# Performance work log

Hardware: AMD Instinct MI355X
Metric: run time of the kernel (lower is better)

Reference implementation:

```python
import jax, jax.numpy as jnp
import numpy as np

NUM_HEADS = 4

def setup_inputs() -> dict:
    key = jax.random.key(0)
    ks = jax.random.split(key, 7)
    B, Lq, Lk, E, D, LAT = 16, 256, 4096, 64, 32, 32
    query = jax.random.normal(ks[0], (B, Lq, E), dtype=jnp.float32)
    key_in = jax.random.normal(ks[1], (B, Lk, E), dtype=jnp.float32)
    value = jax.random.normal(ks[2], (B, Lk, D), dtype=jnp.float32)
    mask = jax.random.randint(ks[3], (B, Lk, D), 0, 2, dtype=jnp.int32)
    Wq = jax.random.normal(ks[4], (E, E), dtype=jnp.float32) / np.sqrt(E).astype(np.float32)
    bq = jnp.zeros((E,), dtype=jnp.float32)
    Wk = jax.random.normal(ks[5], (E, E), dtype=jnp.float32) / np.sqrt(E).astype(np.float32)
    bk = jnp.zeros((E,), dtype=jnp.float32)
    Wo = jax.random.normal(ks[6], (NUM_HEADS * D, LAT), dtype=jnp.float32) / np.sqrt(NUM_HEADS * D).astype(np.float32)
    bo = jnp.zeros((LAT,), dtype=jnp.float32)
    return {"query": query, "key": key_in, "value": value, "mask": mask,
            "Wq": Wq, "bq": bq, "Wk": Wk, "bk": bk, "Wo": Wo, "bo": bo}

def reference(query, key, value, mask, Wq, bq, Wk, bk, Wo, bo):
    B, Lk, D = value.shape
    Lq = query.shape[1]
    h = NUM_HEADS
    ek = query.shape[-1] // h  # embed_time_k
    # linear maps (torch Linear: y = x @ W; here W stored as (in, out))
    q = (query @ Wq + bq).reshape(B, Lq, h, ek).transpose(0, 2, 1, 3)  # (B,h,Lq,ek)
    k = (key @ Wk + bk).reshape(B, Lk, h, ek).transpose(0, 2, 1, 3)    # (B,h,Lk,ek)
    scores = jnp.einsum('bhqe,bhke->bhqk', q, k) / jnp.sqrt(jnp.asarray(ek, q.dtype))
    # Original repeats scores over D, masks per-feature with -inf, softmaxes over Lk,
    # then does a weighted sum. Equivalent fused form (never builds (B,h,Lq,Lk,D)):
    e = jnp.exp(scores - jnp.max(scores, axis=-1, keepdims=True))  # (B,h,Lq,Lk)
    m = mask.astype(value.dtype)                                   # (B,Lk,D) 0/1
    num = jnp.einsum('bhqk,bkd->bhqd', e, m * value)
    den = jnp.einsum('bhqk,bkd->bhqd', e, m)
    x = num / den                                                  # (B,h,Lq,D)
    x = x.transpose(0, 2, 1, 3).reshape(B, Lq, h * D)
    return x @ Wo + bo  # (B, Lq, latent_dim)
```

## Files before the change

kernel.cpp:

```cpp
#include <hip/hip_runtime.h>
#include <hip/hip_bf16.h>
#include <math.h>

typedef __bf16 bf16;
typedef bf16 bf16x2 __attribute__((ext_vector_type(2)));
typedef bf16 bf16x4 __attribute__((ext_vector_type(4)));
typedef bf16 bf16x8 __attribute__((ext_vector_type(8)));
typedef float f32x4 __attribute__((ext_vector_type(4)));
typedef float f32x16 __attribute__((ext_vector_type(16)));
typedef unsigned int u32x2 __attribute__((ext_vector_type(2)));
typedef unsigned int u32x4 __attribute__((ext_vector_type(4)));

#define B_   16
#define LQ_  256
#define LK_  4096
#define E_   64
#define H_   4
#define EK_  16
#define D_   32
#define LAT_ 32

#define OFF_QP    0u
#define OFF_KP    524288u
#define OFF_MVFB  8912896u
#define OFF_WOT   17301504u
#define OFF_NDP   17309696u
#define WS_NEED   50864128u

#define LOG2E 1.44269504f

__device__ inline f32x4 mfma_bf16(bf16x8 a, bf16x8 b, f32x4 c) {
  return __builtin_amdgcn_mfma_f32_16x16x32_bf16(a, b, c, 0, 0, 0);
}
__device__ inline f32x16 mfma_bf16_32(bf16x8 a, bf16x8 b, f32x16 c) {
  return __builtin_amdgcn_mfma_f32_32x32x16_bf16(a, b, c, 0, 0, 0);
}

__device__ inline void pl32swap(unsigned &a, unsigned &b) {
#if __has_builtin(__builtin_amdgcn_permlane32_swap)
  u32x2 r = __builtin_amdgcn_permlane32_swap(a, b, false, false);
  a = r[0]; b = r[1];
#else
  asm volatile("v_permlane32_swap_b32 %0, %1" : "+v"(a), "+v"(b));
#endif
}

__global__ __launch_bounds__(256) void prep_kernel(
    const float* __restrict__ query, const float* __restrict__ key,
    const float* __restrict__ value, const int* __restrict__ mask,
    const float* __restrict__ Wq, const float* __restrict__ bq,
    const float* __restrict__ Wk, const float* __restrict__ bk,
    const float* __restrict__ Wo,
    bf16* __restrict__ qp, bf16* __restrict__ kp,
    bf16* __restrict__ mvfB, bf16* __restrict__ WoT)
{
  __shared__ __align__(16) bf16 s_b[16896];
  const int bid = blockIdx.x;
  const int tid = threadIdx.x;

  if (bid < 544) {
    const bool isQ = bid < 32;
    const int row0 = isQ ? bid * 128 : (bid - 32) * 128;
    const float* in   = isQ ? query : key;
    const float* W    = isQ ? Wq : Wk;
    const float* bias = isQ ? bq : bk;
    bf16* outp        = isQ ? qp : kp;
    const float scal  = isQ ? (0.25f * LOG2E) : 1.0f;

    bf16* sIn = s_b;
    bf16* sWT = s_b + 9216;

#pragma unroll
    for (int p = 0; p < 8; ++p) {
      int f4 = tid + p * 256;
      int row = f4 >> 4, e4 = (f4 & 15) * 4;
      float4 v = *(const float4*)(in + (size_t)(row0 + row) * 64 + e4);
      bf16x4 b4;
      b4[0] = (bf16)v.x; b4[1] = (bf16)v.y; b4[2] = (bf16)v.z; b4[3] = (bf16)v.w;
      *(bf16x4*)(sIn + row * 72 + e4) = b4;
    }
#pragma unroll
    for (int p = 0; p < 4; ++p) {
      int f4 = tid + p * 256;
      int k = f4 >> 4, c4 = (f4 & 15) * 4;
      float4 v = *(const float4*)(W + k * 64 + c4);
      sWT[(c4 + 0) * 72 + k] = (bf16)v.x;
      sWT[(c4 + 1) * 72 + k] = (bf16)v.y;
      sWT[(c4 + 2) * 72 + k] = (bf16)v.z;
      sWT[(c4 + 3) * 72 + k] = (bf16)v.w;
    }
    __syncthreads();

    const int w = tid >> 6, l = tid & 63, l15 = l & 15, g = l >> 4;
    f32x4 acc[2][4];
#pragma unroll
    for (int mt = 0; mt < 2; ++mt)
#pragma unroll
      for (int nt = 0; nt < 4; ++nt) acc[mt][nt] = f32x4{0.f, 0.f, 0.f, 0.f};

#pragma unroll
    for (int ks = 0; ks < 2; ++ks) {
      bf16x8 A0 = *(bf16x8*)(sIn + (32 * w + l15) * 72 + 32 * ks + 8 * g);
      bf16x8 A1 = *(bf16x8*)(sIn + (32 * w + 16 + l15) * 72 + 32 * ks + 8 * g);
#pragma unroll
      for (int nt = 0; nt < 4; ++nt) {
        bf16x8 Bf = *(bf16x8*)(sWT + (16 * nt + l15) * 72 + 32 * ks + 8 * g);
        acc[0][nt] = mfma_bf16(A0, Bf, acc[0][nt]);
        acc[1][nt] = mfma_bf16(A1, Bf, acc[1][nt]);
      }
    }
#pragma unroll
    for (int mt = 0; mt < 2; ++mt)
#pragma unroll
      for (int nt = 0; nt < 4; ++nt) {
        int col = 16 * nt + l15;
        float bv = bias[col];
#pragma unroll
        for (int r = 0; r < 4; ++r) {
          int row = row0 + 32 * w + 16 * mt + 4 * g + r;
          outp[(size_t)row * 64 + col] = (bf16)((acc[mt][nt][r] + bv) * scal);
        }
      }
  } else if (bid < 800) {
    const int rb = bid - 544;
    const int b = rb >> 4, kk0 = (rb & 15) * 256;
#pragma unroll
    for (int p = 0; p < 8; ++p) {
      int f4 = tid + p * 256;
      int kk = f4 >> 3, d4 = (f4 & 7) * 4;
      size_t gi = ((size_t)(b * LK_ + kk0 + kk)) * 32 + d4;
      float4 v = *(const float4*)(value + gi);
      int4   m = *(const int4*)(mask + gi);
      s_b[(d4 + 0) * 264 + kk] = (bf16)(m.x ? v.x : 0.0f);
      s_b[(d4 + 1) * 264 + kk] = (bf16)(m.y ? v.y : 0.0f);
      s_b[(d4 + 2) * 264 + kk] = (bf16)(m.z ? v.z : 0.0f);
      s_b[(d4 + 3) * 264 + kk] = (bf16)(m.w ? v.w : 0.0f);
      s_b[(32 + d4 + 0) * 264 + kk] = (bf16)(float)m.x;
      s_b[(32 + d4 + 1) * 264 + kk] = (bf16)(float)m.y;
      s_b[(32 + d4 + 2) * 264 + kk] = (bf16)(float)m.z;
      s_b[(32 + d4 + 3) * 264 + kk] = (bf16)(float)m.w;
    }
    __syncthreads();
    const int col = tid >> 2, seg = tid & 3;
    const int nd = col >> 5, n31 = col & 31;
#pragma unroll
    for (int w2 = 0; w2 < 8; ++w2) {
      int kkg = seg * 64 + w2 * 8;
      int tile = (kk0 + kkg) >> 5;
      int ks   = (kkg >> 4) & 1;
      int hi2  = (kkg >> 3) & 1;
      int lane = n31 + 32 * hi2;
      uint4 d = *(uint4*)(s_b + col * 264 + kkg);
      *(uint4*)(mvfB + (size_t)((((b * 128 + tile) * 2 + ks) * 2 + nd) * 64 + lane) * 8) = d;
    }
  } else {
#pragma unroll
    for (int p = 0; p < 16; ++p) {
      int f = tid + p * 256;
      int k = f >> 5, n = f & 31;
      WoT[n * 128 + k] = (bf16)Wo[f];
    }
  }
}

__global__ __launch_bounds__(256, 4) void attn_kernel(
    const bf16* __restrict__ qp, const bf16* __restrict__ kp,
    const bf16* __restrict__ mvfB, float* __restrict__ ndp)
{
  const int bid = blockIdx.x;
  const int kc = bid & 7, qt = (bid >> 3) & 7, b = bid >> 6;
  const int tid = threadIdx.x;
  const int h = tid >> 6, l = tid & 63;
  const int l31 = l & 31, hi = l >> 5;
  const int q0 = qt * 32;
  const int tile0 = kc * 16;

  bf16x8 qB = *(const bf16x8*)(qp + (size_t)((b * LQ_ + q0 + l31) * 64 + h * EK_ + hi * 8));

  f32x16 accN, accD, Z;
#pragma unroll
  for (int i = 0; i < 16; ++i) { accN[i] = 0.f; accD[i] = 0.f; Z[i] = 0.f; }

  const bf16* mvt0 = mvfB + (size_t)(b * 128 + tile0) * 2048;
  const bf16* kp_b = kp + (size_t)(b * LK_ + tile0 * 32) * 64 + h * EK_ + hi * 8;

#pragma unroll 2
  for (int t = 0; t < 16; ++t) {
    const bf16* mvt = mvt0 + (size_t)t * 2048;

    bf16x8 Bn0 = *(const bf16x8*)(mvt + (0 * 64 + l) * 8);
    bf16x8 Bd0 = *(const bf16x8*)(mvt + (1 * 64 + l) * 8);
    bf16x8 Bn1 = *(const bf16x8*)(mvt + (2 * 64 + l) * 8);
    bf16x8 Bd1 = *(const bf16x8*)(mvt + (3 * 64 + l) * 8);

    bf16x8 kA = *(const bf16x8*)(kp_b + (size_t)(t * 32 + l31) * 64);

    f32x16 S = mfma_bf16_32(kA, qB, Z);

    unsigned P[8];
#pragma unroll
    for (int i = 0; i < 8; ++i) {
      union { bf16x2 hh; unsigned u; } cv;
      cv.hh[0] = (bf16)exp2f(S[2 * i + 0]);
      cv.hh[1] = (bf16)exp2f(S[2 * i + 1]);
      P[i] = cv.u;
    }
    pl32swap(P[0], P[2]);
    pl32swap(P[1], P[3]);
    pl32swap(P[4], P[6]);
    pl32swap(P[5], P[7]);
    union { u32x4 u; bf16x8 v; } pa0, pa1;
    pa0.u = (u32x4){P[0], P[1], P[2], P[3]};
    pa1.u = (u32x4){P[4], P[5], P[6], P[7]};

    accN = mfma_bf16_32(pa0.v, Bn0, accN);
    accD = mfma_bf16_32(pa0.v, Bd0, accD);
    accN = mfma_bf16_32(pa1.v, Bn1, accN);
    accD = mfma_bf16_32(pa1.v, Bd1, accD);
  }

  float* ndp_w = ndp + ((((size_t)kc * B_ + b) * H_ + h) * LQ_ + q0) * 64;
#pragma unroll
  for (int r = 0; r < 16; ++r) {
    int q = (r & 3) + 8 * (r >> 2) + 4 * hi;
    ndp_w[(size_t)q * 64 + l31]      = accN[r];
    ndp_w[(size_t)q * 64 + 32 + l31] = accD[r];
  }
}

__global__ __launch_bounds__(256) void out_kernel(
    const float* __restrict__ ndp, const bf16* __restrict__ WoT,
    const float* __restrict__ bo, float* __restrict__ out)
{
  __shared__ __align__(16) bf16 s_x[16 * 136];
  const int bid = blockIdx.x;
  const int b = bid >> 4, q0 = (bid & 15) * 16;
  const int tid = threadIdx.x;
  const int q = tid >> 4, jg = tid & 15;
  const int h = jg >> 2, d0 = (jg & 3) * 8;

  f32x4 nlo = f32x4{0.f,0.f,0.f,0.f}, nhi = f32x4{0.f,0.f,0.f,0.f};
  f32x4 dlo = f32x4{0.f,0.f,0.f,0.f}, dhi = f32x4{0.f,0.f,0.f,0.f};
#pragma unroll
  for (int kc = 0; kc < 8; ++kc) {
    const float* p = ndp + ((((size_t)kc * B_ + b) * H_ + h) * LQ_ + q0 + q) * 64;
    nlo += *(const f32x4*)(p + d0);
    nhi += *(const f32x4*)(p + d0 + 4);
    dlo += *(const f32x4*)(p + 32 + d0);
    dhi += *(const f32x4*)(p + 32 + d0 + 4);
  }
  bf16* sx = s_x + q * 136 + h * 32 + d0;
#pragma unroll
  for (int i = 0; i < 4; ++i) {
    sx[i]     = (bf16)(nlo[i] / dlo[i]);
    sx[4 + i] = (bf16)(nhi[i] / dhi[i]);
  }
  __syncthreads();
  const int w = tid >> 6, l = tid & 63, l15 = l & 15, g = l >> 4;
  if (w < 2) {
    const int nt = w;
    f32x4 acc = f32x4{0.f, 0.f, 0.f, 0.f};
#pragma unroll
    for (int ks = 0; ks < 4; ++ks) {
      bf16x8 A  = *(bf16x8*)(s_x + l15 * 136 + 32 * ks + 8 * g);
      bf16x8 Bf = *(const bf16x8*)(WoT + (l15 + 16 * nt) * 128 + 32 * ks + 8 * g);
      acc = mfma_bf16(A, Bf, acc);
    }
    float bv = bo[l15 + 16 * nt];
#pragma unroll
    for (int r = 0; r < 4; ++r) {
      int row = q0 + 4 * g + r;
      out[(size_t)(b * LQ_ + row) * LAT_ + l15 + 16 * nt] = acc[r] + bv;
    }
  }
}

extern "C" void kernel_launch(void* const* d_in, const int* in_sizes, int n_in,
                              void* d_out, int out_size, void* d_ws, size_t ws_size,
                              hipStream_t stream) {
  const float* query = (const float*)d_in[0];
  const float* key   = (const float*)d_in[1];
  const float* value = (const float*)d_in[2];
  const int*   mask  = (const int*)d_in[3];
  const float* Wq    = (const float*)d_in[4];
  const float* bq    = (const float*)d_in[5];
  const float* Wk    = (const float*)d_in[6];
  const float* bk    = (const float*)d_in[7];
  const float* Wo    = (const float*)d_in[8];
  const float* bo    = (const float*)d_in[9];
  float* out = (float*)d_out;
  char* ws = (char*)d_ws;

  if (ws_size < (size_t)WS_NEED) return;

  bf16* qp   = (bf16*)(ws + OFF_QP);
  bf16* kp   = (bf16*)(ws + OFF_KP);
  bf16* mvfB = (bf16*)(ws + OFF_MVFB);
  bf16* WoT  = (bf16*)(ws + OFF_WOT);
  float* ndp = (float*)(ws + OFF_NDP);

  prep_kernel<<<801, 256, 0, stream>>>(query, key, value, mask, Wq, bq, Wk, bk,
                                       Wo, qp, kp, mvfB, WoT);
  attn_kernel<<<1024, 256, 0, stream>>>(qp, kp, mvfB, ndp);
  out_kernel<<<256, 256, 0, stream>>>(ndp, WoT, bo, out);
}
```

Baseline: 125.9 us.

## Fuse split-K reduction and output projection into attention kernel via last-block counter

Removes the separate output kernel. Each (batch, query-tile) group keeps an atomic counter, reset in the prep kernel. The last of its 8 key-chunk blocks sums the partial numerators and denominators, divides them, and runs the Wo projection with MFMA. This saves one kernel launch and its dependency gap, at the cost of threadfences, an atomic per block, and extra LDS in the attention kernel that may lower occupancy.

```diff
diff --git a/kernel.cpp b/kernel.cpp
--- a/kernel.cpp
+++ b/kernel.cpp
@@ -25,7 +25,8 @@
 #define OFF_MVFB  8912896u
 #define OFF_WOT   17301504u
 #define OFF_NDP   17309696u
-#define WS_NEED   50864128u
+#define OFF_CNT   50864128u
+#define WS_NEED   50864640u
 
 #define LOG2E 1.44269504f
 
@@ -52,7 +53,7 @@
     const float* __restrict__ Wk, const float* __restrict__ bk,
     const float* __restrict__ Wo,
     bf16* __restrict__ qp, bf16* __restrict__ kp,
-    bf16* __restrict__ mvfB, bf16* __restrict__ WoT)
+    bf16* __restrict__ mvfB, bf16* __restrict__ WoT, int* __restrict__ cnt)
 {
   __shared__ __align__(16) bf16 s_b[16896];
   const int bid = blockIdx.x;
@@ -160,13 +161,19 @@
       int k = f >> 5, n = f & 31;
       WoT[n * 128 + k] = (bf16)Wo[f];
     }
+    if (tid < 128) cnt[tid] = 0;
   }
 }
 
 __global__ __launch_bounds__(256, 4) void attn_kernel(
     const bf16* __restrict__ qp, const bf16* __restrict__ kp,
-    const bf16* __restrict__ mvfB, float* __restrict__ ndp)
+    const bf16* __restrict__ mvfB, float* __restrict__ ndp,
+    const bf16* __restrict__ WoT, const float* __restrict__ bo,
+    float* __restrict__ out, int* __restrict__ cnt)
 {
+  __shared__ __align__(16) bf16 s_x[32 * 136];
+  __shared__ int sLast;
+
   const int bid = blockIdx.x;
   const int kc = bid & 7, qt = (bid >> 3) & 7, b = bid >> 6;
   const int tid = threadIdx.x;
@@ -226,51 +233,60 @@
     ndp_w[(size_t)q * 64 + l31]      = accN[r];
     ndp_w[(size_t)q * 64 + 32 + l31] = accD[r];
   }
-}
-
-__global__ __launch_bounds__(256) void out_kernel(
-    const float* __restrict__ ndp, const bf16* __restrict__ WoT,
-    const float* __restrict__ bo, float* __restrict__ out)
-{
-  __shared__ __align__(16) bf16 s_x[16 * 136];
-  const int bid = blockIdx.x;
-  const int b = bid >> 4, q0 = (bid & 15) * 16;
-  const int tid = threadIdx.x;
-  const int q = tid >> 4, jg = tid & 15;
-  const int h = jg >> 2, d0 = (jg & 3) * 8;
-
-  f32x4 nlo = f32x4{0.f,0.f,0.f,0.f}, nhi = f32x4{0.f,0.f,0.f,0.f};
-  f32x4 dlo = f32x4{0.f,0.f,0.f,0.f}, dhi = f32x4{0.f,0.f,0.f,0.f};
-#pragma unroll
-  for (int kc = 0; kc < 8; ++kc) {
-    const float* p = ndp + ((((size_t)kc * B_ + b) * H_ + h) * LQ_ + q0 + q) * 64;
-    nlo += *(const f32x4*)(p + d0);
-    nhi += *(const f32x4*)(p + d0 + 4);
-    dlo += *(const f32x4*)(p + 32 + d0);
-    dhi += *(const f32x4*)(p + 32 + d0 + 4);
-  }
-  bf16* sx = s_x + q * 136 + h * 32 + d0;
-#pragma unroll
-  for (int i = 0; i < 4; ++i) {
-    sx[i]     = (bf16)(nlo[i] / dlo[i]);
-    sx[4 + i] = (bf16)(nhi[i] / dhi[i]);
-  }
+
   __syncthreads();
-  const int w = tid >> 6, l = tid & 63, l15 = l & 15, g = l >> 4;
-  if (w < 2) {
-    const int nt = w;
-    f32x4 acc = f32x4{0.f, 0.f, 0.f, 0.f};
+  if (tid == 0) {
+    __threadfence();
+    sLast = (atomicAdd(&cnt[b * 8 + qt], 1) == 7);
+  }
+  __syncthreads();
+  if (!sLast) return;
+  __threadfence();
+  __syncthreads();
+
+  {
+    const int q = tid >> 3, s = tid & 7;
+    const int hh = s >> 1, dh = (s & 1) * 16;
+    f32x4 n0 = f32x4{0.f,0.f,0.f,0.f}, n1 = n0, n2 = n0, n3 = n0;
+    f32x4 e0 = n0, e1 = n0, e2 = n0, e3 = n0;
+#pragma unroll
+    for (int k = 0; k < 8; ++k) {
+      const float* p = ndp + ((((size_t)k * B_ + b) * H_ + hh) * LQ_ + q0 + q) * 64 + dh;
+      n0 += *(const f32x4*)(p + 0);
+      n1 += *(const f32x4*)(p + 4);
+      n2 += *(const f32x4*)(p + 8);
+      n3 += *(const f32x4*)(p + 12);
+      e0 += *(const f32x4*)(p + 32 + 0);
+      e1 += *(const f32x4*)(p + 32 + 4);
+      e2 += *(const f32x4*)(p + 32 + 8);
+      e3 += *(const f32x4*)(p + 32 + 12);
+    }
+    bf16* sx = s_x + q * 136 + hh * 32 + dh;
+#pragma unroll
+    for (int i = 0; i < 4; ++i) {
+      sx[i]      = (bf16)(n0[i] / e0[i]);
+      sx[4 + i]  = (bf16)(n1[i] / e1[i]);
+      sx[8 + i]  = (bf16)(n2[i] / e2[i]);
+      sx[12 + i] = (bf16)(n3[i] / e3[i]);
+    }
+  }
+  __syncthreads();
+
+  {
+    const int w = tid >> 6, l15 = l & 15, g = (l >> 4) & 3;
+    const int mq = w >> 1, nt = w & 1;
+    f32x4 acc2 = f32x4{0.f, 0.f, 0.f, 0.f};
 #pragma unroll
     for (int ks = 0; ks < 4; ++ks) {
-      bf16x8 A  = *(bf16x8*)(s_x + l15 * 136 + 32 * ks + 8 * g);
-      bf16x8 Bf = *(const bf16x8*)(WoT + (l15 + 16 * nt) * 128 + 32 * ks + 8 * g);
-      acc = mfma_bf16(A, Bf, acc);
-    }
-    float bv = bo[l15 + 16 * nt];
+      bf16x8 A  = *(bf16x8*)(s_x + (16 * mq + l15) * 136 + 32 * ks + 8 * g);
+      bf16x8 Bf = *(const bf16x8*)(WoT + (16 * nt + l15) * 128 + 32 * ks + 8 * g);
+      acc2 = mfma_bf16(A, Bf, acc2);
+    }
+    float bv = bo[16 * nt + l15];
 #pragma unroll
     for (int r = 0; r < 4; ++r) {
-      int row = q0 + 4 * g + r;
-      out[(size_t)(b * LQ_ + row) * LAT_ + l15 + 16 * nt] = acc[r] + bv;
+      int row = q0 + 16 * mq + 4 * g + r;
+      out[(size_t)(b * LQ_ + row) * LAT_ + 16 * nt + l15] = acc2[r] + bv;
     }
   }
 }
@@ -298,9 +314,9 @@
   bf16* mvfB = (bf16*)(ws + OFF_MVFB);
   bf16* WoT  = (bf16*)(ws + OFF_WOT);
   float* ndp = (float*)(ws + OFF_NDP);
+  int*   cnt = (int*)(ws + OFF_CNT);
 
   prep_kernel<<<801, 256, 0, stream>>>(query, key, value, mask, Wq, bq, Wk, bk,
-                                       Wo, qp, kp, mvfB, WoT);
-  attn_kernel<<<1024, 256, 0, stream>>>(qp, kp, mvfB, ndp);
-  out_kernel<<<256, 256, 0, stream>>>(ndp, WoT, bo, out);
-}
+                                       Wo, qp, kp, mvfB, WoT, cnt);
+  attn_kernel<<<1024, 256, 0, stream>>>(qp, kp, mvfB, ndp, WoT, bo, out, cnt);
+}
```

Result: slower. 197.2 us (+56.7%).
